# Kernel tuning notes

Hardware: AMD Instinct MI355X
Metric: run time of the kernel (lower is better)

Reference implementation:

```python
import jax, jax.numpy as jnp
import numpy as np

NUM_HEADS = 8
NUM_GROUPS = 8
EPS = 1e-5


def setup_inputs() -> dict:
    key = jax.random.key(0)
    ks = jax.random.split(key, 4)
    B, C, H, W = 16, 512, 32, 32
    x = jax.random.normal(ks[0], (B, C, H, W), dtype=jnp.float32)
    gamma = jnp.ones((C,), jnp.float32)
    beta = jnp.zeros((C,), jnp.float32)
    w_qkv = jax.random.normal(ks[1], (3 * C, C), jnp.float32) * (1.0 / np.sqrt(C))
    b_qkv = jnp.zeros((3 * C,), jnp.float32)
    w_out = jax.random.normal(ks[2], (C, C), jnp.float32) * (1.0 / np.sqrt(C))
    b_out = jnp.zeros((C,), jnp.float32)
    return {"x": x, "gamma": gamma, "beta": beta, "w_qkv": w_qkv,
            "b_qkv": b_qkv, "w_out": w_out, "b_out": b_out}


def _group_norm(x, gamma, beta):
    b, c, h, w = x.shape
    xg = x.reshape(b, NUM_GROUPS, c // NUM_GROUPS, h, w)
    mean = xg.mean(axis=(2, 3, 4), keepdims=True)
    var = xg.var(axis=(2, 3, 4), keepdims=True)
    xn = ((xg - mean) * jax.lax.rsqrt(var + EPS)).reshape(b, c, h, w)
    return xn * gamma[None, :, None, None] + beta[None, :, None, None]


def reference(x, gamma, beta, w_qkv, b_qkv, w_out, b_out):
    b, c, h, w = x.shape
    hd = c // NUM_HEADS
    scale = hd ** -0.5
    xn = _group_norm(x, gamma, beta)
    # 1x1 conv == per-pixel linear: (3c, c) x (b, c, h, w) -> (b, 3c, h, w)
    qkv = jnp.einsum('oc,bchw->bohw', w_qkv, xn) + b_qkv[None, :, None, None]
    q, k, v = jnp.split(qkv, 3, axis=1)
    q = q.reshape(b, NUM_HEADS, hd, h * w)
    k = k.reshape(b, NUM_HEADS, hd, h * w)
    v = v.reshape(b, NUM_HEADS, hd, h * w)
    attn = jnp.einsum('bhdi,bhdj->bhij', q, k) * scale  # (b, heads, hw, hw)
    attn = jax.nn.softmax(attn, axis=-1)
    out = jnp.einsum('bhij,bhdj->bhdi', attn, v).reshape(b, c, h, w)
    out = jnp.einsum('oc,bchw->bohw', w_out, out) + b_out[None, :, None, None]
    return x + out
```

## Files before the change

### kernel.cpp

```cpp
#include <hip/hip_runtime.h>
#include <hip/hip_bf16.h>

#define BB   16
#define CCH  512
#define PP   1024
#define NHD  8

typedef unsigned short u16;
typedef unsigned int   u32;
typedef __attribute__((ext_vector_type(8))) short bf16x8;
typedef __attribute__((ext_vector_type(4))) float f32x4;

__device__ __forceinline__ u16 f2bu(float f) {
    __hip_bfloat16 h = __float2bfloat16(f);
    return *reinterpret_cast<u16*>(&h);
}

__launch_bounds__(256)
__global__ void pre_k(const float* __restrict__ x,
                      float* __restrict__ ps, float* __restrict__ pss,
                      const float* __restrict__ w1, const float* __restrict__ w2,
                      u16* __restrict__ d1, u16* __restrict__ d2) {
    int blk = blockIdx.x;
    if (blk < 512) {
        int bg = blk >> 2, part = blk & 3;
        const float4* xp = (const float4*)(x + (size_t)bg * 65536 + (size_t)part * 16384);
        float s = 0.f, ss = 0.f;
        for (int i = threadIdx.x; i < 4096; i += 256) {
            float4 v = xp[i];
            s  += v.x + v.y + v.z + v.w;
            ss += v.x*v.x + v.y*v.y + v.z*v.z + v.w*v.w;
        }
        __shared__ float sh[256], sq[256];
        sh[threadIdx.x] = s; sq[threadIdx.x] = ss;
        __syncthreads();
        for (int off = 128; off > 0; off >>= 1) {
            if (threadIdx.x < off) {
                sh[threadIdx.x] += sh[threadIdx.x + off];
                sq[threadIdx.x] += sq[threadIdx.x + off];
            }
            __syncthreads();
        }
        if (threadIdx.x == 0) {
            ps[blk]  = sh[0];
            pss[blk] = sq[0];
        }
    } else {
        int id = (blk - 512) * 256 + threadIdx.x;
        const float* s; u16* d; int off;
        if (id < 196608) { s = w1; d = d1; off = id * 4; }
        else             { s = w2; d = d2; off = (id - 196608) * 4; }
        float4 v = *(const float4*)(s + off);
        ushort4 o;
        o.x = f2bu(v.x); o.y = f2bu(v.y); o.z = f2bu(v.z); o.w = f2bu(v.w);
        *(ushort4*)(d + off) = o;
    }
}

__launch_bounds__(256)
__global__ void conv_x_k(const float* __restrict__ x,
                         const float* __restrict__ ps, const float* __restrict__ pss,
                         const float* __restrict__ gamma, const float* __restrict__ beta,
                         u16* __restrict__ xbt) {
    __shared__ u16 T[64][73];
    const int tid = threadIdx.x;
    const int p0 = blockIdx.x * 64;
    const int c0 = blockIdx.y * 64;
    const int b  = blockIdx.z;
    const int bg = (b << 3) + (c0 >> 6);
    float s4  = ps[bg*4]  + ps[bg*4+1]  + ps[bg*4+2]  + ps[bg*4+3];
    float ss4 = pss[bg*4] + pss[bg*4+1] + pss[bg*4+2] + pss[bg*4+3];
    float m   = s4 * (1.f / 65536.f);
    float var = ss4 * (1.f / 65536.f) - m * m;
    float rs  = rsqrtf(var + 1e-5f);
    {
        int ci = tid >> 2, psx = (tid & 3) * 16;
        int c = c0 + ci;
        float sc = rs * gamma[c];
        float sf = beta[c] - m * sc;
        const float* xp = x + ((size_t)(b * CCH + c)) * PP + p0 + psx;
        #pragma unroll
        for (int j4 = 0; j4 < 4; j4++) {
            float4 v = *(const float4*)(xp + j4 * 4);
            T[psx + j4*4 + 0][ci] = f2bu(v.x * sc + sf);
            T[psx + j4*4 + 1][ci] = f2bu(v.y * sc + sf);
            T[psx + j4*4 + 2][ci] = f2bu(v.z * sc + sf);
            T[psx + j4*4 + 3][ci] = f2bu(v.w * sc + sf);
        }
    }
    __syncthreads();
    {
        int pi = tid >> 2, cs = (tid & 3) * 16;
        u16* dst = xbt + ((size_t)(b * PP) + p0 + pi) * CCH + c0 + cs;
        #pragma unroll
        for (int j4 = 0; j4 < 4; j4++) {
            ushort4 o;
            o.x = T[pi][cs + j4*4 + 0]; o.y = T[pi][cs + j4*4 + 1];
            o.z = T[pi][cs + j4*4 + 2]; o.w = T[pi][cs + j4*4 + 3];
            *(ushort4*)(dst + j4 * 4) = o;
        }
    }
}

__launch_bounds__(256)
__global__ void mgemm_qkv_k(const u16* __restrict__ Wb, const float* __restrict__ bias,
                            const u16* __restrict__ actT,
                            u16* __restrict__ qT, u16* __restrict__ kT,
                            u16* __restrict__ v) {
    __shared__ __align__(16) u16 smem[17408];
    u16* As = smem;
    u16* Bs = smem + 5120;
    const int tid = threadIdx.x;
    const int id = blockIdx.x;
    const int wk = (id & 7) * 192 + (id >> 3);
    const int b  = wk / 96;
    const int wi = wk % 96;
    const int m0 = (wi >> 3) * 128;
    const int p0 = (wi & 7) * 128;
    const int w = tid >> 6, l = tid & 63, quad = l >> 4, lm = l & 15;
    const int mo = (w >> 1) * 64, no = (w & 1) * 64;

    f32x4 acc[4][4] = {};

    const int srow = tid >> 1, sks = (tid & 1) << 4;
    const u16* wp = Wb + (size_t)(m0 + srow) * CCH + sks;
    const u16* ap = actT + (size_t)b * PP * CCH + (size_t)(p0 + srow) * CCH + sks;
    u16* asw = &As[srow * 40 + sks];
    u16* bsw = &Bs[srow * 40 + sks];

    uint4 aw0 = *(const uint4*)(wp);
    uint4 aw1 = *(const uint4*)(wp + 8);
    uint4 bw0 = *(const uint4*)(ap);
    uint4 bw1 = *(const uint4*)(ap + 8);

    for (int k0 = 0; k0 < CCH; k0 += 32) {
        *(uint4*)asw = aw0;  *(uint4*)(asw + 8) = aw1;
        *(uint4*)bsw = bw0;  *(uint4*)(bsw + 8) = bw1;
        __syncthreads();
        if (k0 + 32 < CCH) {
            aw0 = *(const uint4*)(wp + k0 + 32);
            aw1 = *(const uint4*)(wp + k0 + 40);
            bw0 = *(const uint4*)(ap + k0 + 32);
            bw1 = *(const uint4*)(ap + k0 + 40);
        }
        bf16x8 af[4], bfr[4];
        #pragma unroll
        for (int mi = 0; mi < 4; mi++)
            af[mi] = *(const bf16x8*)&As[(mo + mi*16 + lm) * 40 + quad * 8];
        #pragma unroll
        for (int ni = 0; ni < 4; ni++)
            bfr[ni] = *(const bf16x8*)&Bs[(no + ni*16 + lm) * 40 + quad * 8];
        __builtin_amdgcn_s_setprio(1);
        #pragma unroll
        for (int mi = 0; mi < 4; mi++)
            #pragma unroll
            for (int ni = 0; ni < 4; ni++)
                acc[mi][ni] = __builtin_amdgcn_mfma_f32_16x16x32_bf16(
                    af[mi], bfr[ni], acc[mi][ni], 0, 0, 0);
        __builtin_amdgcn_s_setprio(0);
        __syncthreads();
    }

    const int region = m0 >> 9;
    if (region < 2) {
        const float scl = (region == 0) ? 0.18033688011f : 1.0f;
        u16* Cb = smem;
        #pragma unroll
        for (int mi = 0; mi < 4; mi++) {
            f32x4 bv = *(const f32x4*)&bias[m0 + mo + mi*16 + quad*4];
            #pragma unroll
            for (int ni = 0; ni < 4; ni++) {
                int colp = no + ni*16 + lm;
                int rowb = mo + mi*16 + quad*4;
                #pragma unroll
                for (int r = 0; r < 4; r++)
                    Cb[colp * 136 + rowb + r] = f2bu((acc[mi][ni][r] + bv[r]) * scl);
            }
        }
        __syncthreads();
        int prow = tid >> 1, half = tid & 1;
        u16* base = (region == 0) ? qT : kT;
        u16* dst = base + ((size_t)b * PP + p0 + prow) * 512 + (m0 & 511) + half * 64;
        const u16* src = &Cb[prow * 136 + half * 64];
        #pragma unroll
        for (int i = 0; i < 8; i++)
            *(uint4*)(dst + i * 8) = *(const uint4*)(src + i * 8);
    } else {
        u16* Cb = smem;
        #pragma unroll
        for (int mi = 0; mi < 4; mi++) {
            f32x4 bv = *(const f32x4*)&bias[m0 + mo + mi*16 + quad*4];
            #pragma unroll
            for (int ni = 0; ni < 4; ni++) {
                int colp = no + ni*16 + lm;
                int rowb = mo + mi*16 + quad*4;
                #pragma unroll
                for (int r = 0; r < 4; r++)
                    Cb[(rowb + r) * 136 + colp] = f2bu(acc[mi][ni][r] + bv[r]);
            }
        }
        __syncthreads();
        int row = tid >> 1, half = tid & 1;
        u16* dst = v + ((size_t)b * 512 + (m0 - 1024) + row) * PP + p0 + half * 64;
        const u16* src = &Cb[row * 136 + half * 64];
        #pragma unroll
        for (int i = 0; i < 8; i++)
            *(uint4*)(dst + i * 8) = *(const uint4*)(src + i * 8);
    }
}

__launch_bounds__(512, 4)
__global__ void fattn_k(const u16* __restrict__ qT, const u16* __restrict__ kT,
                        const u16* __restrict__ v, u16* __restrict__ ao) {
    __shared__ __align__(16) u16 Ps[128 * 136];
    __shared__ __align__(16) u16 Ks[128 * 72];
    __shared__ __align__(16) u16 Vs[64 * 136];
    const int tid = threadIdx.x;
    const int id = blockIdx.x;
    const int wk = ((id & 7) << 7) | (id >> 3);
    const int q0 = (wk & 7) * 128;
    const int pair = wk >> 3;
    const int h = pair & 7;
    const int b = pair >> 3;
    const int w = tid >> 6, l = tid & 63, quad = l >> 4, lm = l & 15;
    const int psw = ((lm >> 2) & 3) << 4;

    {
        int r = w * 16 + (l >> 2), c = (l & 3) * 16;
        int swz = ((l >> 4) & 3) << 4;
        const u16* src = qT + ((size_t)b * PP + q0 + r) * 512 + h * 64 + c;
        *(uint4*)&Ps[r * 136 + (c ^ swz)]     = *(const uint4*)src;
        *(uint4*)&Ps[r * 136 + (c ^ swz) + 8] = *(const uint4*)(src + 8);
    }
    bf16x8 qf0 = *(const bf16x8*)&Ps[(w * 16 + lm) * 136 + ((quad * 8) ^ psw)];
    bf16x8 qf1 = *(const bf16x8*)&Ps[(w * 16 + lm) * 136 + ((32 + quad * 8) ^ psw)];

    bf16x8 onesv;
    #pragma unroll
    for (int i = 0; i < 8; i++) onesv[i] = (short)0x3F80;

    f32x4 O[4] = {};
    f32x4 Ol = {};

    const int ksr = tid >> 2, ksc = (tid & 3) * 16;
    const int vsr = tid >> 3, vsc = (tid & 7) * 16;

    uint4 ka, kb, va, vb;
    {
        const u16* ksrc = kT + ((size_t)b * PP + ksr) * 512 + h * 64 + ksc;
        ka = *(const uint4*)ksrc; kb = *(const uint4*)(ksrc + 8);
        const u16* vsrc = v + ((size_t)b * 512 + h * 64 + vsr) * PP + vsc;
        va = *(const uint4*)vsrc; vb = *(const uint4*)(vsrc + 8);
    }

    for (int j0 = 0; j0 < PP; j0 += 128) {
        __syncthreads();
        *(uint4*)&Ks[ksr * 72 + ksc]      = ka;
        *(uint4*)&Ks[ksr * 72 + ksc + 8]  = kb;
        *(uint4*)&Vs[vsr * 136 + vsc]     = va;
        *(uint4*)&Vs[vsr * 136 + vsc + 8] = vb;
        __syncthreads();

        if (j0 + 128 < PP) {
            const u16* ksrc = kT + ((size_t)b * PP + j0 + 128 + ksr) * 512 + h * 64 + ksc;
            ka = *(const uint4*)ksrc; kb = *(const uint4*)(ksrc + 8);
            const u16* vsrc = v + ((size_t)b * 512 + h * 64 + vsr) * PP + j0 + 128 + vsc;
            va = *(const uint4*)vsrc; vb = *(const uint4*)(vsrc + 8);
        }

        f32x4 s[8];
        __builtin_amdgcn_s_setprio(1);
        #pragma unroll
        for (int ni = 0; ni < 8; ni++) {
            bf16x8 kf0 = *(const bf16x8*)&Ks[(ni*16 + lm) * 72 + quad * 8];
            bf16x8 kf1 = *(const bf16x8*)&Ks[(ni*16 + lm) * 72 + 32 + quad * 8];
            f32x4 z = {};
            z = __builtin_amdgcn_mfma_f32_16x16x32_bf16(qf0, kf0, z, 0, 0, 0);
            s[ni] = __builtin_amdgcn_mfma_f32_16x16x32_bf16(qf1, kf1, z, 0, 0, 0);
        }
        __builtin_amdgcn_s_setprio(0);

        #pragma unroll
        for (int r = 0; r < 4; r++) {
            int rowb = (w * 16 + quad * 4 + r) * 136 + lm;
            #pragma unroll
            for (int ni = 0; ni < 8; ni++) {
                float p = __builtin_amdgcn_exp2f(s[ni][r]);
                Ps[rowb + 16 * (ni ^ quad)] = f2bu(p);
            }
        }

        __builtin_amdgcn_s_setprio(1);
        #pragma unroll
        for (int kf = 0; kf < 4; kf++) {
            bf16x8 pf = *(const bf16x8*)&Ps[(w*16 + lm) * 136 + ((kf * 32 + quad * 8) ^ psw)];
            Ol = __builtin_amdgcn_mfma_f32_16x16x32_bf16(pf, onesv, Ol, 0, 0, 0);
            #pragma unroll
            for (int nd = 0; nd < 4; nd++) {
                bf16x8 vf = *(const bf16x8*)&Vs[(nd*16 + lm) * 136 + kf * 32 + quad * 8];
                O[nd] = __builtin_amdgcn_mfma_f32_16x16x32_bf16(pf, vf, O[nd], 0, 0, 0);
            }
        }
        __builtin_amdgcn_s_setprio(0);
    }

    #pragma unroll
    for (int r = 0; r < 4; r++) {
        float rinv = 1.f / Ol[r];
        int rowb = (w * 16 + quad * 4 + r) * 136 + lm;
        Ps[rowb + 16 * (0 ^ quad)] = f2bu(O[0][r] * rinv);
        Ps[rowb + 16 * (1 ^ quad)] = f2bu(O[1][r] * rinv);
        Ps[rowb + 16 * (2 ^ quad)] = f2bu(O[2][r] * rinv);
        Ps[rowb + 16 * (3 ^ quad)] = f2bu(O[3][r] * rinv);
    }
    {
        int r = w * 16 + (l >> 2), c = (l & 3) * 16;
        int swz = ((l >> 4) & 3) << 4;
        u16* dst = ao + ((size_t)b * PP + q0 + r) * 512 + h * 64 + c;
        *(uint4*)dst       = *(const uint4*)&Ps[r * 136 + (c ^ swz)];
        *(uint4*)(dst + 8) = *(const uint4*)&Ps[r * 136 + (c ^ swz) + 8];
    }
}

__launch_bounds__(256)
__global__ void mgemm_out_k(const u16* __restrict__ Wb, const float* __restrict__ bias,
                            const u16* __restrict__ actT, const float* __restrict__ resid,
                            float* __restrict__ out) {
    __shared__ __align__(16) u16 smem[10240];
    u16* As = smem;
    u16* Bs = smem + 5120;
    const int tid = threadIdx.x;
    const int id = blockIdx.x;
    const int wk = (id & 7) * 64 + (id >> 3);
    const int b  = wk >> 5;
    const int wi = wk & 31;
    const int m0 = (wi >> 3) * 128;
    const int p0 = (wi & 7) * 128;
    const int w = tid >> 6, l = tid & 63, quad = l >> 4, lm = l & 15;
    const int mo = (w >> 1) * 64, no = (w & 1) * 64;

    f32x4 acc[4][4] = {};

    const int srow = tid >> 1, sks = (tid & 1) << 4;
    const u16* wp = Wb + (size_t)(m0 + srow) * CCH + sks;
    const u16* ap = actT + (size_t)b * PP * CCH + (size_t)(p0 + srow) * CCH + sks;
    u16* asw = &As[srow * 40 + sks];
    u16* bsw = &Bs[srow * 40 + sks];

    uint4 aw0 = *(const uint4*)(wp);
    uint4 aw1 = *(const uint4*)(wp + 8);
    uint4 bw0 = *(const uint4*)(ap);
    uint4 bw1 = *(const uint4*)(ap + 8);

    for (int k0 = 0; k0 < CCH; k0 += 32) {
        *(uint4*)asw = aw0;  *(uint4*)(asw + 8) = aw1;
        *(uint4*)bsw = bw0;  *(uint4*)(bsw + 8) = bw1;
        __syncthreads();
        if (k0 + 32 < CCH) {
            aw0 = *(const uint4*)(wp + k0 + 32);
            aw1 = *(const uint4*)(wp + k0 + 40);
            bw0 = *(const uint4*)(ap + k0 + 32);
            bw1 = *(const uint4*)(ap + k0 + 40);
        }
        bf16x8 af[4], bfr[4];
        #pragma unroll
        for (int mi = 0; mi < 4; mi++)
            af[mi] = *(const bf16x8*)&As[(mo + mi*16 + lm) * 40 + quad * 8];
        #pragma unroll
        for (int ni = 0; ni < 4; ni++)
            bfr[ni] = *(const bf16x8*)&Bs[(no + ni*16 + lm) * 40 + quad * 8];
        __builtin_amdgcn_s_setprio(1);
        #pragma unroll
        for (int mi = 0; mi < 4; mi++)
            #pragma unroll
            for (int ni = 0; ni < 4; ni++)
                acc[mi][ni] = __builtin_amdgcn_mfma_f32_16x16x32_bf16(
                    af[mi], bfr[ni], acc[mi][ni], 0, 0, 0);
        __builtin_amdgcn_s_setprio(0);
        __syncthreads();
    }

    #pragma unroll
    for (int mi = 0; mi < 4; mi++) {
        f32x4 bv = *(const f32x4*)&bias[m0 + mo + mi*16 + quad*4];
        #pragma unroll
        for (int ni = 0; ni < 4; ni++) {
            int p = p0 + no + ni*16 + lm;
            #pragma unroll
            for (int r = 0; r < 4; r++) {
                int m = m0 + mo + mi*16 + quad*4 + r;
                size_t idx = ((size_t)b * CCH + m) * PP + p;
                out[idx] = acc[mi][ni][r] + bv[r] + resid[idx];
            }
        }
    }
}

extern "C" void kernel_launch(void* const* d_in, const int* in_sizes, int n_in,
                              void* d_out, int out_size, void* d_ws, size_t ws_size,
                              hipStream_t stream) {
    const float* x     = (const float*)d_in[0];
    const float* gamma = (const float*)d_in[1];
    const float* beta  = (const float*)d_in[2];
    const float* w_qkv = (const float*)d_in[3];
    const float* b_qkv = (const float*)d_in[4];
    const float* w_out = (const float*)d_in[5];
    const float* b_out = (const float*)d_in[6];

    char* ws = (char*)d_ws;
    float* ps  = (float*)ws;
    float* pss = (float*)(ws + 2048);
    u16* wqb = (u16*)(ws + 4096);
    u16* wob = wqb + 1536 * 512;
    u16* xbt = wob + 512 * 512;
    u16* ao  = xbt + (size_t)BB * PP * CCH;
    u16* qTb = ao  + (size_t)BB * PP * CCH;
    u16* kTb = qTb + (size_t)BB * PP * CCH;
    u16* vb  = kTb + (size_t)BB * PP * CCH;

    pre_k<<<1536, 256, 0, stream>>>(x, ps, pss, w_qkv, w_out, wqb, wob);
    conv_x_k<<<dim3(16, 8, 16), 256, 0, stream>>>(x, ps, pss, gamma, beta, xbt);
    mgemm_qkv_k<<<1536, 256, 0, stream>>>(wqb, b_qkv, xbt, qTb, kTb, vb);
    fattn_k<<<1024, 512, 0, stream>>>(qTb, kTb, vb, ao);
    mgemm_out_k<<<512, 256, 0, stream>>>(wob, b_out, ao, x, (float*)d_out);
}
```

Measured before the change: 235.6 us.

## Use direct global-to-LDS loads with XOR swizzle and K=64 tiles in GEMMs

```diff
diff --git a/kernel.cpp b/kernel.cpp
--- a/kernel.cpp
+++ b/kernel.cpp
@@ -15,6 +15,11 @@
     __hip_bfloat16 h = __float2bfloat16(f);
     return *reinterpret_cast<u16*>(&h);
 }
+
+#define GLOAD_LDS16(gsrc, ldst)                                              \
+    __builtin_amdgcn_global_load_lds(                                        \
+        (const __attribute__((address_space(1))) u32*)(gsrc),                \
+        (__attribute__((address_space(3))) u32*)(ldst), 16, 0, 0)
 
 __launch_bounds__(256)
 __global__ void pre_k(const float* __restrict__ x,
@@ -109,7 +114,7 @@
                             u16* __restrict__ v) {
     __shared__ __align__(16) u16 smem[17408];
     u16* As = smem;
-    u16* Bs = smem + 5120;
+    u16* Bs = smem + 8192;
     const int tid = threadIdx.x;
     const int id = blockIdx.x;
     const int wk = (id & 7) * 192 + (id >> 3);
@@ -122,42 +127,40 @@
 
     f32x4 acc[4][4] = {};
 
-    const int srow = tid >> 1, sks = (tid & 1) << 4;
-    const u16* wp = Wb + (size_t)(m0 + srow) * CCH + sks;
-    const u16* ap = actT + (size_t)b * PP * CCH + (size_t)(p0 + srow) * CCH + sks;
-    u16* asw = &As[srow * 40 + sks];
-    u16* bsw = &Bs[srow * 40 + sks];
-
-    uint4 aw0 = *(const uint4*)(wp);
-    uint4 aw1 = *(const uint4*)(wp + 8);
-    uint4 bw0 = *(const uint4*)(ap);
-    uint4 bw1 = *(const uint4*)(ap + 8);
-
-    for (int k0 = 0; k0 < CCH; k0 += 32) {
-        *(uint4*)asw = aw0;  *(uint4*)(asw + 8) = aw1;
-        *(uint4*)bsw = bw0;  *(uint4*)(bsw + 8) = bw1;
-        __syncthreads();
-        if (k0 + 32 < CCH) {
-            aw0 = *(const uint4*)(wp + k0 + 32);
-            aw1 = *(const uint4*)(wp + k0 + 40);
-            bw0 = *(const uint4*)(ap + k0 + 32);
-            bw1 = *(const uint4*)(ap + k0 + 40);
-        }
-        bf16x8 af[4], bfr[4];
-        #pragma unroll
-        for (int mi = 0; mi < 4; mi++)
-            af[mi] = *(const bf16x8*)&As[(mo + mi*16 + lm) * 40 + quad * 8];
-        #pragma unroll
-        for (int ni = 0; ni < 4; ni++)
-            bfr[ni] = *(const bf16x8*)&Bs[(no + ni*16 + lm) * 40 + quad * 8];
-        __builtin_amdgcn_s_setprio(1);
-        #pragma unroll
-        for (int mi = 0; mi < 4; mi++)
+    const int srow = (w << 3) + (l >> 3);
+    const int scc  = ((l & 7) ^ ((l >> 3) & 7)) << 3;
+    const u16* wp = Wb + (size_t)(m0 + srow) * CCH + scc;
+    const u16* ap = actT + (size_t)b * PP * CCH + (size_t)(p0 + srow) * CCH + scc;
+    const int ldsrow = ((w << 3)) * 64;
+
+    const int c0a = (quad ^ (lm & 7)) << 3;
+
+    for (int k0 = 0; k0 < CCH; k0 += 64) {
+        #pragma unroll
+        for (int is = 0; is < 4; is++) {
+            GLOAD_LDS16(wp + k0 + (size_t)(is * 32) * CCH, &As[is * 2048 + ldsrow]);
+            GLOAD_LDS16(ap + k0 + (size_t)(is * 32) * CCH, &Bs[is * 2048 + ldsrow]);
+        }
+        __syncthreads();
+        #pragma unroll
+        for (int hf = 0; hf < 2; hf++) {
+            const int cofs = hf ? (c0a ^ 32) : c0a;
+            bf16x8 af[4], bfr[4];
+            #pragma unroll
+            for (int mi = 0; mi < 4; mi++)
+                af[mi] = *(const bf16x8*)&As[(mo + mi*16 + lm) * 64 + cofs];
             #pragma unroll
             for (int ni = 0; ni < 4; ni++)
-                acc[mi][ni] = __builtin_amdgcn_mfma_f32_16x16x32_bf16(
-                    af[mi], bfr[ni], acc[mi][ni], 0, 0, 0);
-        __builtin_amdgcn_s_setprio(0);
+                bfr[ni] = *(const bf16x8*)&Bs[(no + ni*16 + lm) * 64 + cofs];
+            __builtin_amdgcn_s_setprio(1);
+            #pragma unroll
+            for (int mi = 0; mi < 4; mi++)
+                #pragma unroll
+                for (int ni = 0; ni < 4; ni++)
+                    acc[mi][ni] = __builtin_amdgcn_mfma_f32_16x16x32_bf16(
+                        af[mi], bfr[ni], acc[mi][ni], 0, 0, 0);
+            __builtin_amdgcn_s_setprio(0);
+        }
         __syncthreads();
     }
 
@@ -326,9 +329,9 @@
 __global__ void mgemm_out_k(const u16* __restrict__ Wb, const float* __restrict__ bias,
                             const u16* __restrict__ actT, const float* __restrict__ resid,
                             float* __restrict__ out) {
-    __shared__ __align__(16) u16 smem[10240];
+    __shared__ __align__(16) u16 smem[16384];
     u16* As = smem;
-    u16* Bs = smem + 5120;
+    u16* Bs = smem + 8192;
     const int tid = threadIdx.x;
     const int id = blockIdx.x;
     const int wk = (id & 7) * 64 + (id >> 3);
@@ -341,42 +344,40 @@
 
     f32x4 acc[4][4] = {};
 
-    const int srow = tid >> 1, sks = (tid & 1) << 4;
-    const u16* wp = Wb + (size_t)(m0 + srow) * CCH + sks;
-    const u16* ap = actT + (size_t)b * PP * CCH + (size_t)(p0 + srow) * CCH + sks;
-    u16* asw = &As[srow * 40 + sks];
-    u16* bsw = &Bs[srow * 40 + sks];
-
-    uint4 aw0 = *(const uint4*)(wp);
-    uint4 aw1 = *(const uint4*)(wp + 8);
-    uint4 bw0 = *(const uint4*)(ap);
-    uint4 bw1 = *(const uint4*)(ap + 8);
-
-    for (int k0 = 0; k0 < CCH; k0 += 32) {
-        *(uint4*)asw = aw0;  *(uint4*)(asw + 8) = aw1;
-        *(uint4*)bsw = bw0;  *(uint4*)(bsw + 8) = bw1;
-        __syncthreads();
-        if (k0 + 32 < CCH) {
-            aw0 = *(const uint4*)(wp + k0 + 32);
-            aw1 = *(const uint4*)(wp + k0 + 40);
-            bw0 = *(const uint4*)(ap + k0 + 32);
-            bw1 = *(const uint4*)(ap + k0 + 40);
-        }
-        bf16x8 af[4], bfr[4];
-        #pragma unroll
-        for (int mi = 0; mi < 4; mi++)
-            af[mi] = *(const bf16x8*)&As[(mo + mi*16 + lm) * 40 + quad * 8];
-        #pragma unroll
-        for (int ni = 0; ni < 4; ni++)
-            bfr[ni] = *(const bf16x8*)&Bs[(no + ni*16 + lm) * 40 + quad * 8];
-        __builtin_amdgcn_s_setprio(1);
-        #pragma unroll
-        for (int mi = 0; mi < 4; mi++)
+    const int srow = (w << 3) + (l >> 3);
+    const int scc  = ((l & 7) ^ ((l >> 3) & 7)) << 3;
+    const u16* wp = Wb + (size_t)(m0 + srow) * CCH + scc;
+    const u16* ap = actT + (size_t)b * PP * CCH + (size_t)(p0 + srow) * CCH + scc;
+    const int ldsrow = ((w << 3)) * 64;
+
+    const int c0a = (quad ^ (lm & 7)) << 3;
+
+    for (int k0 = 0; k0 < CCH; k0 += 64) {
+        #pragma unroll
+        for (int is = 0; is < 4; is++) {
+            GLOAD_LDS16(wp + k0 + (size_t)(is * 32) * CCH, &As[is * 2048 + ldsrow]);
+            GLOAD_LDS16(ap + k0 + (size_t)(is * 32) * CCH, &Bs[is * 2048 + ldsrow]);
+        }
+        __syncthreads();
+        #pragma unroll
+        for (int hf = 0; hf < 2; hf++) {
+            const int cofs = hf ? (c0a ^ 32) : c0a;
+            bf16x8 af[4], bfr[4];
+            #pragma unroll
+            for (int mi = 0; mi < 4; mi++)
+                af[mi] = *(const bf16x8*)&As[(mo + mi*16 + lm) * 64 + cofs];
             #pragma unroll
             for (int ni = 0; ni < 4; ni++)
-                acc[mi][ni] = __builtin_amdgcn_mfma_f32_16x16x32_bf16(
-                    af[mi], bfr[ni], acc[mi][ni], 0, 0, 0);
-        __builtin_amdgcn_s_setprio(0);
+                bfr[ni] = *(const bf16x8*)&Bs[(no + ni*16 + lm) * 64 + cofs];
+            __builtin_amdgcn_s_setprio(1);
+            #pragma unroll
+            for (int mi = 0; mi < 4; mi++)
+                #pragma unroll
+                for (int ni = 0; ni < 4; ni++)
+                    acc[mi][ni] = __builtin_amdgcn_mfma_f32_16x16x32_bf16(
+                        af[mi], bfr[ni], acc[mi][ni], 0, 0, 0);
+            __builtin_amdgcn_s_setprio(0);
+        }
         __syncthreads();
     }
 
```

Measured after the change: 231.2 us. About the same (-1.9%).
